# Performance work log

Hardware: AMD Instinct MI355X
Metric: run time of the kernel (lower is better)

Reference implementation:

```python
import jax, jax.numpy as jnp
import numpy as np

ROW_DIMS = (8, 10, 20, 20)   # factorization of vocab = 32000
COL_DIMS = (4, 4, 6, 8)      # factorization of out_features = 768
RANKS = (1, 16, 16, 16, 1)
VOCAB = int(np.prod(ROW_DIMS))
OUT = int(np.prod(COL_DIMS))
# cum_prod[k] = prod(ROW_DIMS[k+1:]) -> mixed-radix digit extraction
CUM_PROD = np.concatenate([np.cumprod(ROW_DIMS[::-1])[::-1][1:], [1]]).astype(np.int32)


def setup_inputs() -> dict:
    key = jax.random.key(0)
    ks = jax.random.split(key, 5)
    x = jax.random.randint(ks[0], (8, 4096), 0, VOCAB, dtype=jnp.int32)
    cores = {}
    for k in range(4):
        shp = (RANKS[k], ROW_DIMS[k], COL_DIMS[k], RANKS[k + 1])
        # scale so that the product of 4 cores has ~unit stddev per element
        std = 1.0 / np.sqrt(RANKS[k + 1])
        cores[f"core{k}"] = (jax.random.normal(ks[k + 1], shp, dtype=jnp.float32) * std)
    return {"x": x, **cores}


def reference(x, core0, core1, core2, core3):
    cores = (core0, core1, core2, core3)
    idx = x.reshape(-1)                 # [B] flattened token indices
    B = idx.shape[0]
    digits = [(idx // CUM_PROD[k]) % ROW_DIMS[k] for k in range(4)]
    # first core: [1, n0, m0, r1] -> gather -> [B, m0, r1]
    res = core0[0][digits[0]].reshape(B, COL_DIMS[0], RANKS[1])
    for k in range(1, 4):
        g = jnp.take(cores[k], digits[k], axis=1)        # [r_k, B, m_k, r_{k+1}]
        res = jnp.einsum('bar,rbms->bams', res, g)       # chain contraction over rank
        res = res.reshape(B, -1, RANKS[k + 1])
    rows = res.reshape(B, OUT)
    return rows.reshape(*x.shape, OUT)
```

## Files before the change

kernel.cpp:

```cpp
#include <hip/hip_runtime.h>


#define NTOK   32768
#define TPW    8
#define G01_BYTES  (80 * 256 * 4)
#define G23_BYTES  (400 * 768 * 4)
#define TBL_BYTES  (G01_BYTES + G23_BYTES)

#define FMA4(A, S, V) { (A).x += (S)*(V).x; (A).y += (S)*(V).y; \
                        (A).z += (S)*(V).z; (A).w += (S)*(V).w; }

__global__ void build_tables(const float* __restrict__ core0,
                             const float* __restrict__ core1,
                             const float* __restrict__ core2,
                             const float* __restrict__ core3,
                             float* __restrict__ g01,
                             float* __restrict__ g23) {
    int b = blockIdx.x;
    int t = threadIdx.x;
    if (b < 400) {
        int d2 = b / 20, d3 = b % 20;
#pragma unroll
        for (int i = 0; i < 3; ++i) {
            int flat = t + i * 256;
            int r2 = flat / 48, mc = flat % 48;
            int m2 = mc >> 3, m3 = mc & 7;
            float acc = 0.f;
#pragma unroll
            for (int r3 = 0; r3 < 16; ++r3) {
                float c2 = core2[((r2 * 20 + d2) * 6 + m2) * 16 + r3];
                float c3 = core3[(r3 * 20 + d3) * 8 + m3];
                acc += c2 * c3;
            }
            g23[b * 768 + flat] = acc;
        }
    } else {
        int combo = b - 400;
        int d0 = combo / 10, d1 = combo % 10;
        int a = t >> 4, r2 = t & 15;
        int a0 = a >> 2, m1 = a & 3;
        float acc = 0.f;
#pragma unroll
        for (int r1 = 0; r1 < 16; ++r1) {
            float c0 = core0[(d0 * 4 + a0) * 16 + r1];
            float c1 = core1[((r1 * 10 + d1) * 4 + m1) * 16 + r2];
            acc += c0 * c1;
        }
        g01[combo * 256 + t] = acc;
    }
}

__global__ __launch_bounds__(256) void te_stream(const int* __restrict__ x,
                                                 const float* __restrict__ g01,
                                                 const float* __restrict__ g23,
                                                 float* __restrict__ out) {
    __shared__ float lds[4][2][768];
    const int wave = threadIdx.x >> 6;
    const int lane = threadIdx.x & 63;
    const int gw = blockIdx.x * 4 + wave;
    const int tok0 = gw * TPW;
    const int a = lane >> 2, q = lane & 3;
    float* __restrict__ b0 = lds[wave][0];
    float* __restrict__ b1 = lds[wave][1];

    int4 xa = ((const int4*)(x + tok0))[0];
    int4 xb = ((const int4*)(x + tok0))[1];
    int idxs[TPW] = {xa.x, xa.y, xa.z, xa.w, xb.x, xb.y, xb.z, xb.w};

    {
        const float4* G2 = (const float4*)(g23 + (idxs[0] % 400) * 768);
        float4 t0 = G2[lane], t1 = G2[lane + 64], t2 = G2[lane + 128];
        ((float4*)b0)[lane] = t0;
        ((float4*)b0)[lane + 64] = t1;
        ((float4*)b0)[lane + 128] = t2;
    }
    const float4* g1p = (const float4*)(g01 + (idxs[0] / 400) * 256 + a * 16);
    float4 s0 = g1p[0], s1 = g1p[1], s2 = g1p[2], s3 = g1p[3];

#pragma unroll
    for (int t = 0; t < TPW; ++t) {
        float* cur = (t & 1) ? b1 : b0;
        float* nxt = (t & 1) ? b0 : b1;

        float4 n0, n1, n2, m0, m1, m2, m3;
        if (t + 1 < TPW) {
            const float4* G2n = (const float4*)(g23 + (idxs[t + 1] % 400) * 768);
            n0 = G2n[lane]; n1 = G2n[lane + 64]; n2 = G2n[lane + 128];
            const float4* g1n = (const float4*)(g01 + (idxs[t + 1] / 400) * 256 + a * 16);
            m0 = g1n[0]; m1 = g1n[1]; m2 = g1n[2]; m3 = g1n[3];
        }

        const float* cq = cur + q * 4;
        float4 sarr[4] = {s0, s1, s2, s3};
        float4 acc0 = {0.f,0.f,0.f,0.f}, acc1 = {0.f,0.f,0.f,0.f}, acc2 = {0.f,0.f,0.f,0.f};
#pragma unroll
        for (int rr = 0; rr < 4; ++rr) {
#pragma unroll
            for (int c = 0; c < 4; ++c) {
                const int r2 = rr * 4 + c;
                float4 v0 = *(const float4*)(cq + r2 * 48);
                float4 v1 = *(const float4*)(cq + r2 * 48 + 16);
                float4 v2 = *(const float4*)(cq + r2 * 48 + 32);
                float sv = (c == 0) ? sarr[rr].x : (c == 1) ? sarr[rr].y
                         : (c == 2) ? sarr[rr].z : sarr[rr].w;
                FMA4(acc0, sv, v0);
                FMA4(acc1, sv, v1);
                FMA4(acc2, sv, v2);
            }
        }

        float4* o4 = (float4*)(out + (size_t)(tok0 + t) * 768);
        o4[a * 12 + q]     = acc0;
        o4[a * 12 + q + 4] = acc1;
        o4[a * 12 + q + 8] = acc2;

        if (t + 1 < TPW) {
            ((float4*)nxt)[lane] = n0;
            ((float4*)nxt)[lane + 64] = n1;
            ((float4*)nxt)[lane + 128] = n2;
            s0 = m0; s1 = m1; s2 = m2; s3 = m3;
        }
    }
}


__global__ void precompute_g01_nf(const float* __restrict__ core0,
                                  const float* __restrict__ core1,
                                  float* __restrict__ g01) {
    int combo = blockIdx.x;
    int t = threadIdx.x;
    int d0 = combo / 10, d1 = combo % 10;
    int a = t >> 4, r2 = t & 15;
    int a0 = a >> 2, m1 = a & 3;
    float acc = 0.f;
#pragma unroll
    for (int r1 = 0; r1 < 16; ++r1)
        acc += core0[(d0 * 4 + a0) * 16 + r1] *
               core1[((r1 * 10 + d1) * 4 + m1) * 16 + r2];
    g01[combo * 256 + t] = acc;
}

__global__ void precompute_g23_nf(const float* __restrict__ core2,
                                  const float* __restrict__ core3,
                                  float* __restrict__ g23) {
    int combo = blockIdx.x;
    int t = threadIdx.x;
    int d2 = combo / 20, d3 = combo % 20;
#pragma unroll
    for (int i = 0; i < 3; ++i) {
        int flat = t + i * 256;
        int r2 = flat / 48, mc = flat % 48;
        int m2 = mc >> 3, m3 = mc & 7;
        float acc = 0.f;
#pragma unroll
        for (int r3 = 0; r3 < 16; ++r3)
            acc += core2[((r2 * 20 + d2) * 6 + m2) * 16 + r3] *
                   core3[(r3 * 20 + d3) * 8 + m3];
        g23[combo * 768 + flat] = acc;
    }
}

__global__ __launch_bounds__(256) void te_main(const int* __restrict__ x,
                                               const float* __restrict__ g01,
                                               const float* __restrict__ g23,
                                               float* __restrict__ out) {
    int wave = threadIdx.x >> 6;
    int lane = threadIdx.x & 63;
    int tok = blockIdx.x * 4 + wave;
    int idx = x[tok];
    const float* __restrict__ G1 = g01 + (idx / 400) * 256;
    const float* __restrict__ G2 = g23 + (idx % 400) * 768;
    float* __restrict__ o = out + (size_t)tok * 768;
#pragma unroll
    for (int p = 0; p < 3; ++p) {
        int base = (p * 64 + lane) * 4;
        int a = base / 48;
        int mc = base - a * 48;
        const float4* g1v = (const float4*)(G1 + a * 16);
        float4 ca = g1v[0], cb = g1v[1], cc = g1v[2], cd = g1v[3];
        float s[16] = {ca.x, ca.y, ca.z, ca.w, cb.x, cb.y, cb.z, cb.w,
                       cc.x, cc.y, cc.z, cc.w, cd.x, cd.y, cd.z, cd.w};
        float4 acc = {0.f, 0.f, 0.f, 0.f};
#pragma unroll
        for (int r2 = 0; r2 < 16; ++r2) {
            float4 v = *(const float4*)(G2 + r2 * 48 + mc);
            acc.x += s[r2] * v.x;
            acc.y += s[r2] * v.y;
            acc.z += s[r2] * v.z;
            acc.w += s[r2] * v.w;
        }
        *(float4*)(o + base) = acc;
    }
}

__global__ void te_direct(const int* __restrict__ x,
                          const float* __restrict__ core0,
                          const float* __restrict__ core1,
                          const float* __restrict__ core2,
                          const float* __restrict__ core3,
                          float* __restrict__ out) {
    int tok = blockIdx.x;
    int lane = threadIdx.x;
    int idx = x[tok];
    int d0 = idx / 4000;
    int rem = idx - d0 * 4000;
    int d1 = rem / 400;
    rem -= d1 * 400;
    int d2 = rem / 20;
    int d3 = rem - d2 * 20;
    float* o = out + (size_t)tok * 768;
    for (int p = 0; p < 3; ++p) {
        int base = (p * 64 + lane) * 4;
        int a = base / 48;
        int mc = base - a * 48;
        int a0 = a >> 2, m1 = a & 3;
        float s[16];
#pragma unroll
        for (int r2 = 0; r2 < 16; ++r2) {
            float acc = 0.f;
            for (int r1 = 0; r1 < 16; ++r1)
                acc += core0[(d0 * 4 + a0) * 16 + r1] *
                       core1[((r1 * 10 + d1) * 4 + m1) * 16 + r2];
            s[r2] = acc;
        }
        float4 accv = {0.f, 0.f, 0.f, 0.f};
        float* accp = (float*)&accv;
        for (int j = 0; j < 4; ++j) {
            int mcj = mc + j;
            int m2 = mcj >> 3, m3 = mcj & 7;
            float tt = 0.f;
            for (int r2 = 0; r2 < 16; ++r2) {
                float g = 0.f;
                for (int r3 = 0; r3 < 16; ++r3)
                    g += core2[((r2 * 20 + d2) * 6 + m2) * 16 + r3] *
                         core3[(r3 * 20 + d3) * 8 + m3];
                tt += s[r2] * g;
            }
            accp[j] = tt;
        }
        *(float4*)(o + base) = accv;
    }
}

extern "C" void kernel_launch(void* const* d_in, const int* in_sizes, int n_in,
                              void* d_out, int out_size, void* d_ws, size_t ws_size,
                              hipStream_t stream) {
    const int*   x     = (const int*)d_in[0];
    const float* core0 = (const float*)d_in[1];
    const float* core1 = (const float*)d_in[2];
    const float* core2 = (const float*)d_in[3];
    const float* core3 = (const float*)d_in[4];
    float* out = (float*)d_out;

    if (ws_size >= (size_t)TBL_BYTES) {
        float* g01 = (float*)d_ws;
        float* g23 = (float*)((char*)d_ws + G01_BYTES);
        build_tables<<<480, 256, 0, stream>>>(core0, core1, core2, core3, g01, g23);
        te_stream<<<NTOK / (4 * TPW), 256, 0, stream>>>(x, g01, g23, out);
    } else {
        te_direct<<<NTOK, 64, 0, stream>>>(x, core0, core1, core2, core3, out);
    }
}
```

Baseline: 31.36 us.

## Stage core slices in LDS for table build and coalesce stream-kernel output stores

The table-building kernel now loads the relevant slices of core0..core3 into shared memory once per block and runs the rank contractions out of LDS, instead of issuing repeated strided global loads. The streaming kernel changes its lane-to-output mapping so each lane writes contiguous float4 positions (lane, lane+64, lane+128). This gives fully coalesced output stores, in exchange for each lane holding three 16-element g01 coefficient vectors (48 extra registers plus a prefetch copy). Unused precompute/te_main kernels are removed.

```diff
diff --git a/kernel.cpp b/kernel.cpp
--- a/kernel.cpp
+++ b/kernel.cpp
@@ -10,42 +10,58 @@
 #define FMA4(A, S, V) { (A).x += (S)*(V).x; (A).y += (S)*(V).y; \
                         (A).z += (S)*(V).z; (A).w += (S)*(V).w; }
 
-__global__ void build_tables(const float* __restrict__ core0,
-                             const float* __restrict__ core1,
-                             const float* __restrict__ core2,
-                             const float* __restrict__ core3,
-                             float* __restrict__ g01,
-                             float* __restrict__ g23) {
+__global__ __launch_bounds__(256) void build_tables(const float* __restrict__ core0,
+                                                    const float* __restrict__ core1,
+                                                    const float* __restrict__ core2,
+                                                    const float* __restrict__ core3,
+                                                    float* __restrict__ g01,
+                                                    float* __restrict__ g23) {
+    __shared__ float s2[1536];
+    __shared__ float s3[128];
+    __shared__ float s1[1024];
+    __shared__ float s0[64];
     int b = blockIdx.x;
     int t = threadIdx.x;
     if (b < 400) {
         int d2 = b / 20, d3 = b % 20;
 #pragma unroll
+        for (int i = 0; i < 6; ++i) {
+            int f = t + i * 256;
+            int r2 = f / 96, j = f - r2 * 96;
+            s2[f] = core2[r2 * 1920 + d2 * 96 + j];
+        }
+        if (t < 128)
+            s3[t] = core3[(t >> 3) * 160 + d3 * 8 + (t & 7)];
+        __syncthreads();
+#pragma unroll
         for (int i = 0; i < 3; ++i) {
-            int flat = t + i * 256;
-            int r2 = flat / 48, mc = flat % 48;
+            int f = t + i * 256;
+            int r2 = f / 48, mc = f - r2 * 48;
             int m2 = mc >> 3, m3 = mc & 7;
             float acc = 0.f;
 #pragma unroll
-            for (int r3 = 0; r3 < 16; ++r3) {
-                float c2 = core2[((r2 * 20 + d2) * 6 + m2) * 16 + r3];
-                float c3 = core3[(r3 * 20 + d3) * 8 + m3];
-                acc += c2 * c3;
-            }
-            g23[b * 768 + flat] = acc;
+            for (int r3 = 0; r3 < 16; ++r3)
+                acc += s2[r2 * 96 + m2 * 16 + r3] * s3[r3 * 8 + m3];
+            g23[b * 768 + f] = acc;
         }
     } else {
         int combo = b - 400;
         int d0 = combo / 10, d1 = combo % 10;
+#pragma unroll
+        for (int i = 0; i < 4; ++i) {
+            int f = t + i * 256;
+            int r1 = f >> 6, j = f & 63;
+            s1[f] = core1[r1 * 640 + d1 * 64 + j];
+        }
+        if (t < 64)
+            s0[t] = core0[d0 * 64 + t];
+        __syncthreads();
         int a = t >> 4, r2 = t & 15;
         int a0 = a >> 2, m1 = a & 3;
         float acc = 0.f;
 #pragma unroll
-        for (int r1 = 0; r1 < 16; ++r1) {
-            float c0 = core0[(d0 * 4 + a0) * 16 + r1];
-            float c1 = core1[((r1 * 10 + d1) * 4 + m1) * 16 + r2];
-            acc += c0 * c1;
-        }
+        for (int r1 = 0; r1 < 16; ++r1)
+            acc += s0[a0 * 16 + r1] * s1[r1 * 64 + m1 * 16 + r2];
         g01[combo * 256 + t] = acc;
     }
 }
@@ -57,139 +73,84 @@
     __shared__ float lds[4][2][768];
     const int wave = threadIdx.x >> 6;
     const int lane = threadIdx.x & 63;
-    const int gw = blockIdx.x * 4 + wave;
-    const int tok0 = gw * TPW;
-    const int a = lane >> 2, q = lane & 3;
+    const int tok0 = (blockIdx.x * 4 + wave) * TPW;
     float* __restrict__ b0 = lds[wave][0];
     float* __restrict__ b1 = lds[wave][1];
+
+    const int sl[3] = {lane, lane + 64, lane + 128};
+    int ap[3], cp[3];
+#pragma unroll
+    for (int p = 0; p < 3; ++p) { ap[p] = sl[p] / 12; cp[p] = sl[p] - ap[p] * 12; }
 
     int4 xa = ((const int4*)(x + tok0))[0];
     int4 xb = ((const int4*)(x + tok0))[1];
     int idxs[TPW] = {xa.x, xa.y, xa.z, xa.w, xb.x, xb.y, xb.z, xb.w};
 
+    float s[3][16];
     {
         const float4* G2 = (const float4*)(g23 + (idxs[0] % 400) * 768);
         float4 t0 = G2[lane], t1 = G2[lane + 64], t2 = G2[lane + 128];
         ((float4*)b0)[lane] = t0;
         ((float4*)b0)[lane + 64] = t1;
         ((float4*)b0)[lane + 128] = t2;
-    }
-    const float4* g1p = (const float4*)(g01 + (idxs[0] / 400) * 256 + a * 16);
-    float4 s0 = g1p[0], s1 = g1p[1], s2 = g1p[2], s3 = g1p[3];
+        const float4* G1 = (const float4*)(g01 + (idxs[0] / 400) * 256);
+#pragma unroll
+        for (int p = 0; p < 3; ++p)
+#pragma unroll
+            for (int k = 0; k < 4; ++k) {
+                float4 r = G1[ap[p] * 4 + k];
+                s[p][k * 4 + 0] = r.x; s[p][k * 4 + 1] = r.y;
+                s[p][k * 4 + 2] = r.z; s[p][k * 4 + 3] = r.w;
+            }
+    }
 
 #pragma unroll
     for (int t = 0; t < TPW; ++t) {
         float* cur = (t & 1) ? b1 : b0;
         float* nxt = (t & 1) ? b0 : b1;
 
-        float4 n0, n1, n2, m0, m1, m2, m3;
+        float4 n0, n1, n2;
+        float m[3][16];
         if (t + 1 < TPW) {
             const float4* G2n = (const float4*)(g23 + (idxs[t + 1] % 400) * 768);
             n0 = G2n[lane]; n1 = G2n[lane + 64]; n2 = G2n[lane + 128];
-            const float4* g1n = (const float4*)(g01 + (idxs[t + 1] / 400) * 256 + a * 16);
-            m0 = g1n[0]; m1 = g1n[1]; m2 = g1n[2]; m3 = g1n[3];
-        }
-
-        const float* cq = cur + q * 4;
-        float4 sarr[4] = {s0, s1, s2, s3};
+            const float4* G1n = (const float4*)(g01 + (idxs[t + 1] / 400) * 256);
+#pragma unroll
+            for (int p = 0; p < 3; ++p)
+#pragma unroll
+                for (int k = 0; k < 4; ++k) {
+                    float4 r = G1n[ap[p] * 4 + k];
+                    m[p][k * 4 + 0] = r.x; m[p][k * 4 + 1] = r.y;
+                    m[p][k * 4 + 2] = r.z; m[p][k * 4 + 3] = r.w;
+                }
+        }
+
         float4 acc0 = {0.f,0.f,0.f,0.f}, acc1 = {0.f,0.f,0.f,0.f}, acc2 = {0.f,0.f,0.f,0.f};
 #pragma unroll
-        for (int rr = 0; rr < 4; ++rr) {
-#pragma unroll
-            for (int c = 0; c < 4; ++c) {
-                const int r2 = rr * 4 + c;
-                float4 v0 = *(const float4*)(cq + r2 * 48);
-                float4 v1 = *(const float4*)(cq + r2 * 48 + 16);
-                float4 v2 = *(const float4*)(cq + r2 * 48 + 32);
-                float sv = (c == 0) ? sarr[rr].x : (c == 1) ? sarr[rr].y
-                         : (c == 2) ? sarr[rr].z : sarr[rr].w;
-                FMA4(acc0, sv, v0);
-                FMA4(acc1, sv, v1);
-                FMA4(acc2, sv, v2);
-            }
+        for (int r2 = 0; r2 < 16; ++r2) {
+            float4 v0 = *(const float4*)(cur + r2 * 48 + cp[0] * 4);
+            float4 v1 = *(const float4*)(cur + r2 * 48 + cp[1] * 4);
+            float4 v2 = *(const float4*)(cur + r2 * 48 + cp[2] * 4);
+            FMA4(acc0, s[0][r2], v0);
+            FMA4(acc1, s[1][r2], v1);
+            FMA4(acc2, s[2][r2], v2);
         }
 
         float4* o4 = (float4*)(out + (size_t)(tok0 + t) * 768);
-        o4[a * 12 + q]     = acc0;
-        o4[a * 12 + q + 4] = acc1;
-        o4[a * 12 + q + 8] = acc2;
+        o4[lane]       = acc0;
+        o4[lane + 64]  = acc1;
+        o4[lane + 128] = acc2;
 
         if (t + 1 < TPW) {
             ((float4*)nxt)[lane] = n0;
             ((float4*)nxt)[lane + 64] = n1;
             ((float4*)nxt)[lane + 128] = n2;
-            s0 = m0; s1 = m1; s2 = m2; s3 = m3;
-        }
-    }
-}
-
-
-__global__ void precompute_g01_nf(const float* __restrict__ core0,
-                                  const float* __restrict__ core1,
-                                  float* __restrict__ g01) {
-    int combo = blockIdx.x;
-    int t = threadIdx.x;
-    int d0 = combo / 10, d1 = combo % 10;
-    int a = t >> 4, r2 = t & 15;
-    int a0 = a >> 2, m1 = a & 3;
-    float acc = 0.f;
-#pragma unroll
-    for (int r1 = 0; r1 < 16; ++r1)
-        acc += core0[(d0 * 4 + a0) * 16 + r1] *
-               core1[((r1 * 10 + d1) * 4 + m1) * 16 + r2];
-    g01[combo * 256 + t] = acc;
-}
-
-__global__ void precompute_g23_nf(const float* __restrict__ core2,
-                                  const float* __restrict__ core3,
-                                  float* __restrict__ g23) {
-    int combo = blockIdx.x;
-    int t = threadIdx.x;
-    int d2 = combo / 20, d3 = combo % 20;
-#pragma unroll
-    for (int i = 0; i < 3; ++i) {
-        int flat = t + i * 256;
-        int r2 = flat / 48, mc = flat % 48;
-        int m2 = mc >> 3, m3 = mc & 7;
-        float acc = 0.f;
-#pragma unroll
-        for (int r3 = 0; r3 < 16; ++r3)
-            acc += core2[((r2 * 20 + d2) * 6 + m2) * 16 + r3] *
-                   core3[(r3 * 20 + d3) * 8 + m3];
-        g23[combo * 768 + flat] = acc;
-    }
-}
-
-__global__ __launch_bounds__(256) void te_main(const int* __restrict__ x,
-                                               const float* __restrict__ g01,
-                                               const float* __restrict__ g23,
-                                               float* __restrict__ out) {
-    int wave = threadIdx.x >> 6;
-    int lane = threadIdx.x & 63;
-    int tok = blockIdx.x * 4 + wave;
-    int idx = x[tok];
-    const float* __restrict__ G1 = g01 + (idx / 400) * 256;
-    const float* __restrict__ G2 = g23 + (idx % 400) * 768;
-    float* __restrict__ o = out + (size_t)tok * 768;
-#pragma unroll
-    for (int p = 0; p < 3; ++p) {
-        int base = (p * 64 + lane) * 4;
-        int a = base / 48;
-        int mc = base - a * 48;
-        const float4* g1v = (const float4*)(G1 + a * 16);
-        float4 ca = g1v[0], cb = g1v[1], cc = g1v[2], cd = g1v[3];
-        float s[16] = {ca.x, ca.y, ca.z, ca.w, cb.x, cb.y, cb.z, cb.w,
-                       cc.x, cc.y, cc.z, cc.w, cd.x, cd.y, cd.z, cd.w};
-        float4 acc = {0.f, 0.f, 0.f, 0.f};
-#pragma unroll
-        for (int r2 = 0; r2 < 16; ++r2) {
-            float4 v = *(const float4*)(G2 + r2 * 48 + mc);
-            acc.x += s[r2] * v.x;
-            acc.y += s[r2] * v.y;
-            acc.z += s[r2] * v.z;
-            acc.w += s[r2] * v.w;
-        }
-        *(float4*)(o + base) = acc;
+#pragma unroll
+            for (int p = 0; p < 3; ++p)
+#pragma unroll
+                for (int k = 0; k < 16; ++k)
+                    s[p][k] = m[p][k];
+        }
     }
 }
 
```

After: 36.91 us. 1.18x slower.
